# Kernel tuning notes

Hardware: AMD Instinct MI355X
Metric: run time of the kernel (lower is better)

The kernel has to match this reference:

```python
import jax, jax.numpy as jnp
import numpy as np

B, T, D, H, d = 2, 2048, 1024, 16, 64
INNER = H * d
SCALE = d ** -0.5


def _rope(x, inv_freq):
    # x: [B, H, T, d], interleaved rotary as in the torch module
    t = x.shape[2]
    pos = jnp.arange(t, dtype=jnp.float32)
    freqs = pos[:, None] * inv_freq[None, :]          # [T, d/2]
    cos_f, sin_f = jnp.cos(freqs), jnp.sin(freqs)
    x1, x2 = x[..., 0::2], x[..., 1::2]
    y1 = x1 * cos_f - x2 * sin_f
    y2 = x1 * sin_f + x2 * cos_f
    return jnp.stack([y1, y2], axis=-1).reshape(x.shape)


def setup_inputs() -> dict:
    key = jax.random.key(0)
    ks = jax.random.split(key, 6)
    x = jax.random.normal(ks[0], (B, T, D), jnp.float32)
    W_qkv = jax.random.normal(ks[1], (D, 3 * INNER), jnp.float32) * (D ** -0.5)
    W_out = jax.random.normal(ks[2], (INNER, D), jnp.float32) * (INNER ** -0.5)
    W_dt = jax.random.normal(ks[3], (D, H), jnp.float32) * 0.01
    b_dt = jnp.full((H,), -4.0, jnp.float32)
    W_gsp = jax.random.normal(ks[4], (D, INNER), jnp.float32) * 0.01
    b_gsp = jnp.full((INNER,), -3.0, jnp.float32)
    inv_freq = 1.0 / (10000.0 ** (jnp.arange(0, d, 2, dtype=jnp.float32) / d))
    return {"x": x, "W_qkv": W_qkv, "W_out": W_out, "W_dt": W_dt,
            "b_dt": b_dt, "W_gsp": W_gsp, "b_gsp": b_gsp, "inv_freq": inv_freq}


def reference(x, W_qkv, W_out, W_dt, b_dt, W_gsp, b_gsp, inv_freq):
    qkv = (x @ W_qkv).reshape(B, T, 3, H, d)
    Q = jnp.moveaxis(qkv[:, :, 0], 1, 2)   # [B,H,T,d]
    K = jnp.moveaxis(qkv[:, :, 1], 1, 2)
    V = jnp.moveaxis(qkv[:, :, 2], 1, 2)
    Q = _rope(Q, inv_freq)
    K = _rope(K, inv_freq)

    dt = jax.nn.softplus(x @ W_dt + b_dt)             # [B,T,H]
    gamma = jnp.moveaxis(jnp.exp(-dt), 1, 2)          # [B,H,T]

    p = jax.nn.sigmoid(x @ W_gsp + b_gsp).reshape(B, T, H, d)
    p = jnp.moveaxis(p, 1, 2)                          # [B,H,T,d]
    gamma_eff = gamma[..., None] * (1.0 - p) + p
    gamma_scalar = gamma_eff.mean(axis=-1)            # [B,H,T]
    V = V * (1.0 - p)

    log_gamma = jnp.log(jnp.clip(gamma_scalar, 1e-6, 1.0 - 1e-6))
    lgc = jnp.cumsum(log_gamma, axis=-1)              # [B,H,T]
    log_D = jnp.clip(lgc[..., :, None] - lgc[..., None, :], -20.0, 0.0)
    causal = jnp.tril(jnp.ones((T, T), jnp.float32))
    Dm = jnp.exp(log_D) * causal                      # [B,H,T,T]

    Wscore = jnp.einsum('bhtd,bhsd->bhts', Q * SCALE, K)
    A = Wscore * Dm
    Y = jnp.einsum('bhts,bhsd->bhtd', A, V)
    Y = jnp.moveaxis(Y, 1, 2).reshape(B, T, INNER)
    return Y @ W_out
```

## Files before the change

### kernel.cpp

```cpp
#include <hip/hip_runtime.h>
#include <hip/hip_bf16.h>
#include <math.h>

#define B_     2
#define T_     2048
#define D_     1024
#define H_     16
#define INNER_ 1024
#define NC_    4224
#define SCALE_ 0.125f

typedef unsigned short u16;
typedef short short8 __attribute__((ext_vector_type(8)));
typedef float f32x4 __attribute__((ext_vector_type(4)));
typedef unsigned short u16x4 __attribute__((ext_vector_type(4)));

__device__ __forceinline__ u16 f2bf(float x) {
  union { float f; unsigned u; } v; v.f = x;
  unsigned r = v.u + 0x7fffu + ((v.u >> 16) & 1u);
  return (u16)(r >> 16);
}
__device__ __forceinline__ float b2f(u16 x) {
  union { unsigned u; float f; } v; v.u = ((unsigned)x) << 16;
  return v.f;
}
__device__ __forceinline__ void gload16(const void* g, void* l) {
  __builtin_amdgcn_global_load_lds(
      (const __attribute__((address_space(1))) void*)g,
      (__attribute__((address_space(3))) void*)l, 16, 0, 0);
}

__global__ __launch_bounds__(256) void cast_bf16_kernel(
    const float* __restrict__ src, u16* __restrict__ dst, int n4) {
  int i = blockIdx.x * 256 + threadIdx.x;
  if (i >= n4) return;
  float4 v = *reinterpret_cast<const float4*>(src + (size_t)i * 4);
  u16x4 o; o.x = f2bf(v.x); o.y = f2bf(v.y); o.z = f2bf(v.z); o.w = f2bf(v.w);
  *reinterpret_cast<u16x4*>(dst + (size_t)i * 4) = o;
}

__global__ __launch_bounds__(256) void cast_transpose_kernel(
    const float* __restrict__ src, u16* __restrict__ dst, int K, int N) {
  __shared__ float tile[64][65];
  const int k0 = blockIdx.y * 64, n0 = blockIdx.x * 64;
  for (int e = threadIdx.x; e < 4096; e += 256) {
    int kk = e >> 6, nn = e & 63;
    tile[kk][nn] = src[(size_t)(k0 + kk) * N + n0 + nn];
  }
  __syncthreads();
  for (int e = threadIdx.x; e < 4096; e += 256) {
    int nn = e >> 6, kk = e & 63;
    dst[(size_t)(n0 + nn) * K + k0 + kk] = f2bf(tile[kk][nn]);
  }
}

__global__ __launch_bounds__(256) void wdt_transpose_kernel(
    const float* __restrict__ W_dt, u16* __restrict__ dst) {
  int i = blockIdx.x * 256 + threadIdx.x;
  int k = i >> 4, h = i & 15;
  dst[(size_t)h * D_ + k] = f2bf(W_dt[i]);
}

__global__ __launch_bounds__(256) void rope_tab_kernel(
    const float* __restrict__ inv_freq, float2* __restrict__ tab) {
  int i = blockIdx.x * 256 + threadIdx.x;
  int t = i >> 5, j = i & 31;
  float s, c;
  sincosf((float)t * inv_freq[j], &s, &c);
  tab[i] = make_float2(c, s);
}

template <bool BF16OUT>
__global__ __launch_bounds__(256) void gemm_bt(
    const u16* __restrict__ A, const u16* __restrict__ Bt,
    void* __restrict__ Cv, int M, int N, int K) {
  __shared__ u16 As[128 * 64] __attribute__((aligned(16)));
  __shared__ u16 Bs[128 * 64] __attribute__((aligned(16)));
  const int tid = threadIdx.x;
  const int w = tid >> 6, l = tid & 63;
  const int m0 = blockIdx.y * 128, n0 = blockIdx.x * 128;
  const int wr = (w >> 1) * 64, wc = (w & 1) * 64;
  const int srow = l >> 3;
  const int kgrp = ((l & 7) ^ srow) * 8;

  f32x4 acc[4][4] = {};

  for (int kt = 0; kt < K; kt += 64) {
    if (kt) __syncthreads();
#pragma unroll
    for (int i = 0; i < 4; ++i) {
      int c = w * 4 + i;
      int row = c * 8 + srow;
      gload16(A + (size_t)(m0 + row) * K + kt + kgrp, (char*)As + c * 1024);
      gload16(Bt + (size_t)(n0 + row) * K + kt + kgrp, (char*)Bs + c * 1024);
    }
    __syncthreads();
#pragma unroll
    for (int kk = 0; kk < 2; ++kk) {
      short8 af[4], bf[4];
#pragma unroll
      for (int i = 0; i < 4; ++i) {
        int ra = wr + i * 16 + (l & 15);
        int sa = kk * 4 + (l >> 4);
        af[i] = *(const short8*)((const char*)As + ra * 128 + ((sa ^ (ra & 7)) << 4));
        int rb = wc + i * 16 + (l & 15);
        bf[i] = *(const short8*)((const char*)Bs + rb * 128 + ((sa ^ (rb & 7)) << 4));
      }
#pragma unroll
      for (int i = 0; i < 4; ++i)
#pragma unroll
        for (int j = 0; j < 4; ++j)
          acc[i][j] = __builtin_amdgcn_mfma_f32_16x16x32_bf16(af[i], bf[j], acc[i][j], 0, 0, 0);
    }
  }
#pragma unroll
  for (int i = 0; i < 4; ++i) {
#pragma unroll
    for (int r = 0; r < 4; ++r) {
      size_t row = (size_t)(m0 + wr + i * 16 + (l >> 4) * 4 + r);
      size_t base = row * N + n0 + wc + (l & 15);
#pragma unroll
      for (int j = 0; j < 4; ++j) {
        if (BF16OUT) ((u16*)Cv)[base + j * 16] = f2bf(acc[i][j][r]);
        else         ((float*)Cv)[base + j * 16] = acc[i][j][r];
      }
    }
  }
}

__global__ __launch_bounds__(256) void pointwise_kernel(
    const u16* __restrict__ C, const float* __restrict__ b_dt,
    const float* __restrict__ b_gsp, const float2* __restrict__ tab,
    u16* __restrict__ Qb, u16* __restrict__ Kb, u16* __restrict__ Vb,
    float* __restrict__ lg) {
  const int row = blockIdx.x * 4 + (threadIdx.x >> 6);
  const int l = threadIdx.x & 63;
  const int b = row >> 11, t = row & (T_ - 1);
  const int h = l >> 2;
  const int dd0 = (l & 3) * 16;
  const int col = h * 64 + dd0;
  const size_t cb = (size_t)row * NC_;

  float dtv = b2f(C[cb + 4096 + h]) + b_dt[h];
  float sp = (dtv > 20.f) ? dtv : log1pf(__expf(dtv));
  const float gh = __expf(-sp);

  const short8* qp = (const short8*)(C + cb + col);
  const short8* kp = (const short8*)(C + cb + 1024 + col);
  const short8* vp = (const short8*)(C + cb + 2048 + col);
  const short8* pp = (const short8*)(C + cb + 3072 + col);
  short8 q0 = qp[0], q1 = qp[1];
  short8 k0 = kp[0], k1 = kp[1];
  short8 v0 = vp[0], v1 = vp[1];
  short8 pr0 = pp[0], pr1 = pp[1];

  float ge = 0.f;
  short8 vo0, vo1;
#pragma unroll
  for (int i = 0; i < 8; ++i) {
    float pv = b2f((u16)pr0[i]) + b_gsp[col + i];
    float p = 1.f / (1.f + __expf(-pv));
    ge += gh * (1.f - p) + p;
    vo0[i] = (short)f2bf(b2f((u16)v0[i]) * (1.f - p));
    float pv1 = b2f((u16)pr1[i]) + b_gsp[col + 8 + i];
    float p1 = 1.f / (1.f + __expf(-pv1));
    ge += gh * (1.f - p1) + p1;
    vo1[i] = (short)f2bf(b2f((u16)v1[i]) * (1.f - p1));
  }
  const size_t hm = (((size_t)(b * H_ + h)) * T_ + t) * 64 + dd0;
  ((short8*)(Vb + hm))[0] = vo0;
  ((short8*)(Vb + hm))[1] = vo1;

  ge += __shfl_xor(ge, 1);
  ge += __shfl_xor(ge, 2);
  if ((l & 3) == 0) {
    float gs = ge * (1.f / 64.f);
    gs = fminf(fmaxf(gs, 1e-6f), 1.f - 1e-6f);
    lg[((size_t)(b * H_ + h)) * T_ + t] = logf(gs);
  }

  short8 qo0, qo1, ko0, ko1;
  const float2* cs = tab + t * 32 + (dd0 >> 1);
#pragma unroll
  for (int m = 0; m < 4; ++m) {
    float2 c0 = cs[m];
    float qa = b2f((u16)q0[2 * m]), qb = b2f((u16)q0[2 * m + 1]);
    qo0[2 * m]     = (short)f2bf((qa * c0.x - qb * c0.y) * SCALE_);
    qo0[2 * m + 1] = (short)f2bf((qa * c0.y + qb * c0.x) * SCALE_);
    float ka = b2f((u16)k0[2 * m]), kb = b2f((u16)k0[2 * m + 1]);
    ko0[2 * m]     = (short)f2bf(ka * c0.x - kb * c0.y);
    ko0[2 * m + 1] = (short)f2bf(ka * c0.y + kb * c0.x);
    float2 c1 = cs[4 + m];
    float qa1 = b2f((u16)q1[2 * m]), qb1 = b2f((u16)q1[2 * m + 1]);
    qo1[2 * m]     = (short)f2bf((qa1 * c1.x - qb1 * c1.y) * SCALE_);
    qo1[2 * m + 1] = (short)f2bf((qa1 * c1.y + qb1 * c1.x) * SCALE_);
    float ka1 = b2f((u16)k1[2 * m]), kb1 = b2f((u16)k1[2 * m + 1]);
    ko1[2 * m]     = (short)f2bf(ka1 * c1.x - kb1 * c1.y);
    ko1[2 * m + 1] = (short)f2bf(ka1 * c1.y + kb1 * c1.x);
  }
  ((short8*)(Qb + hm))[0] = qo0; ((short8*)(Qb + hm))[1] = qo1;
  ((short8*)(Kb + hm))[0] = ko0; ((short8*)(Kb + hm))[1] = ko1;
}

__global__ __launch_bounds__(256) void scan_kernel(
    const float* __restrict__ lg, float* __restrict__ lgc) {
  const size_t base = (size_t)blockIdx.x * T_;
  const int tid = threadIdx.x;
  __shared__ float sums[256];
  float loc[8];
  float run = 0.f;
#pragma unroll
  for (int i = 0; i < 8; ++i) { run += lg[base + tid * 8 + i]; loc[i] = run; }
  sums[tid] = run;
  __syncthreads();
  if (tid == 0) {
    float r = 0.f;
    for (int i = 0; i < 256; ++i) { float v = sums[i]; sums[i] = r; r += v; }
  }
  __syncthreads();
  const float off = sums[tid];
#pragma unroll
  for (int i = 0; i < 8; ++i) lgc[base + tid * 8 + i] = off + loc[i];
}

__global__ __launch_bounds__(256) void kv_prep_kernel(
    const u16* __restrict__ Kb, const u16* __restrict__ Vb,
    const float* __restrict__ lgc, u16* __restrict__ Kp,
    u16* __restrict__ Vtg) {
  const int stile = blockIdx.x;
  const int bh = blockIdx.y;
  const int tid = threadIdx.x;
  __shared__ u16 vt[64][72];
  const size_t base = ((size_t)bh * T_ + (size_t)stile * 64) * 64;
  const float* lgp = lgc + (size_t)bh * T_;
  const float lgb = lgp[stile * 64];
#pragma unroll
  for (int i = 0; i < 2; ++i) {
    int c = tid * 2 + i;
    int row = c >> 3, k8 = (c & 7) * 8;
    float beta = __expf(lgb - lgp[stile * 64 + row]);
    short8 kv = *(const short8*)(Kb + base + row * 64 + k8);
    short8 ko;
#pragma unroll
    for (int j = 0; j < 8; ++j) ko[j] = (short)f2bf(b2f((u16)kv[j]) * beta);
    *(short8*)(Kp + base + row * 64 + k8) = ko;
    short8 vv = *(const short8*)(Vb + base + row * 64 + k8);
#pragma unroll
    for (int j = 0; j < 8; ++j) vt[row][k8 + j] = (u16)vv[j];
  }
  __syncthreads();
#pragma unroll
  for (int i = 0; i < 2; ++i) {
    int c = tid * 2 + i;
    int dd = c >> 3, t8 = (c & 7) * 8;
    short8 o;
#pragma unroll
    for (int j = 0; j < 8; ++j) o[j] = (short)vt[t8 + j][dd];
    *(short8*)(Vtg + ((size_t)bh * 64 + dd) * T_ + stile * 64 + t8) = o;
  }
}

__global__ __launch_bounds__(256) void attn_mfma(
    const u16* __restrict__ Qb, const u16* __restrict__ Kp,
    const u16* __restrict__ Vtg, const float* __restrict__ lgc,
    u16* __restrict__ Y) {
  const int i = blockIdx.x;
  const int tt = (i >> 3) & 31;
  const int bh = (i & 7) + ((i >> 8) << 3);
  const int b = bh >> 4, h = bh & 15;
  const int tid = threadIdx.x, w = tid >> 6, l = tid & 63;
  __shared__ u16 Qs[64 * 64] __attribute__((aligned(16)));
  __shared__ u16 Ks[64 * 64] __attribute__((aligned(16)));
  __shared__ u16 Vs[64 * 64] __attribute__((aligned(16)));
  const u16* Qg = Qb + (size_t)bh * T_ * 64;
  const u16* Kg = Kp + (size_t)bh * T_ * 64;
  const u16* Vg = Vtg + (size_t)bh * 64 * T_;
  const float* lgp = lgc + (size_t)bh * T_;

  const int srow = l >> 3;
  const int kgrp = ((l & 7) ^ srow) * 8;
  const int ql = l & 15, g4 = l >> 4;

#pragma unroll
  for (int i2 = 0; i2 < 2; ++i2) {
    int c = w * 2 + i2;
    int row = c * 8 + srow;
    gload16(Qg + (size_t)(tt * 64 + row) * 64 + kgrp, (char*)Qs + c * 1024);
  }
  const float lgq = lgp[tt * 64 + w * 16 + ql];
  const float lgtop = lgp[tt * 64];
  __syncthreads();

  short8 qf[2];
#pragma unroll
  for (int kk = 0; kk < 2; ++kk) {
    int row = w * 16 + ql;
    int slot = kk * 4 + g4;
    qf[kk] = *(const short8*)((const char*)Qs + row * 128 + ((slot ^ (row & 7)) << 4));
  }
  char* Pw = (char*)Qs + w * 2048;
  const int pswz = (ql & 7) << 4;

  f32x4 yacc[4] = {};

  for (int st = tt; st >= 0; --st) {
    if (st < tt && lgtop - lgp[st * 64 + 63] <= -20.f) break;
    __syncthreads();
#pragma unroll
    for (int i2 = 0; i2 < 2; ++i2) {
      int c = w * 2 + i2;
      int row = c * 8 + srow;
      gload16(Kg + (size_t)(st * 64 + row) * 64 + kgrp, (char*)Ks + c * 1024);
      gload16(Vg + (size_t)row * T_ + st * 64 + kgrp, (char*)Vs + c * 1024);
    }
    const float alpha = __expf(lgq - lgp[st * 64]);
    __syncthreads();

    const bool diag = (st == tt);
#pragma unroll
    for (int n = 0; n < 4; ++n) {
      f32x4 s = {};
#pragma unroll
      for (int kk = 0; kk < 2; ++kk) {
        int row = n * 16 + ql;
        int slot = kk * 4 + g4;
        short8 kf = *(const short8*)((const char*)Ks + row * 128 + ((slot ^ (row & 7)) << 4));
        s = __builtin_amdgcn_mfma_f32_16x16x32_bf16(kf, qf[kk], s, 0, 0, 0);
      }
      u16x4 pk;
#pragma unroll
      for (int r = 0; r < 4; ++r) {
        float pv = s[r] * alpha;
        if (diag && (n * 16 + g4 * 4 + r) > (w * 16 + ql)) pv = 0.f;
        pk[r] = f2bf(pv);
      }
      *(u16x4*)(Pw + ((ql * 128 + n * 32 + g4 * 8) ^ pswz)) = pk;
    }
#pragma unroll
    for (int kk = 0; kk < 2; ++kk) {
      short8 pf = *(const short8*)(Pw + ((ql * 128 + kk * 64 + g4 * 16) ^ pswz));
#pragma unroll
      for (int n2 = 0; n2 < 4; ++n2) {
        int row = n2 * 16 + ql;
        int slot = kk * 4 + g4;
        short8 vf = *(const short8*)((const char*)Vs + row * 128 + ((slot ^ (row & 7)) << 4));
        yacc[n2] = __builtin_amdgcn_mfma_f32_16x16x32_bf16(pf, vf, yacc[n2], 0, 0, 0);
      }
    }
  }

#pragma unroll
  for (int n2 = 0; n2 < 4; ++n2)
#pragma unroll
    for (int r = 0; r < 4; ++r) {
      size_t row = (size_t)(b * T_) + tt * 64 + w * 16 + g4 * 4 + r;
      Y[row * INNER_ + h * 64 + n2 * 16 + ql] = f2bf(yacc[n2][r]);
    }
}

extern "C" void kernel_launch(void* const* d_in, const int* in_sizes, int n_in,
                              void* d_out, int out_size, void* d_ws, size_t ws_size,
                              hipStream_t stream) {
  const float* x        = (const float*)d_in[0];
  const float* W_qkv    = (const float*)d_in[1];
  const float* W_out    = (const float*)d_in[2];
  const float* W_dt     = (const float*)d_in[3];
  const float* b_dt     = (const float*)d_in[4];
  const float* W_gsp    = (const float*)d_in[5];
  const float* b_gsp    = (const float*)d_in[6];
  const float* inv_freq = (const float*)d_in[7];
  float* out = (float*)d_out;

  const int M = B_ * T_;
  char* p = (char*)d_ws;
  auto alloc = [&](size_t bytes) {
    char* r = p; p += (bytes + 255) & ~(size_t)255; return r;
  };
  u16*    xb    = (u16*)alloc((size_t)M * D_ * 2);
  u16*    Wcombt= (u16*)alloc((size_t)NC_ * D_ * 2);
  u16*    Woutt = (u16*)alloc((size_t)D_ * INNER_ * 2);
  u16*    Cqkvp = (u16*)alloc((size_t)M * NC_ * 2);
  u16*    Qb    = (u16*)alloc((size_t)B_ * H_ * T_ * 64 * 2);
  u16*    Kb    = (u16*)alloc((size_t)B_ * H_ * T_ * 64 * 2);
  u16*    Vb    = (u16*)alloc((size_t)B_ * H_ * T_ * 64 * 2);
  float*  lg    = (float*)alloc((size_t)B_ * H_ * T_ * 4);
  float*  lgc   = (float*)alloc((size_t)B_ * H_ * T_ * 4);
  float2* tab   = (float2*)alloc((size_t)T_ * 32 * 8);
  u16*    Kp    = Cqkvp;
  u16*    Vtg   = Cqkvp + (size_t)4 * 1024 * 1024;
  u16*    Yb    = Cqkvp + (size_t)8 * 1024 * 1024;

  cast_bf16_kernel<<<(M * D_ / 4 + 255) / 256, 256, 0, stream>>>(x, xb, M * D_ / 4);
  rope_tab_kernel<<<T_ * 32 / 256, 256, 0, stream>>>(inv_freq, tab);
  cast_transpose_kernel<<<dim3(3 * INNER_ / 64, D_ / 64), 256, 0, stream>>>(
      W_qkv, Wcombt, D_, 3 * INNER_);
  cast_transpose_kernel<<<dim3(INNER_ / 64, D_ / 64), 256, 0, stream>>>(
      W_gsp, Wcombt + (size_t)3 * INNER_ * D_, D_, INNER_);
  wdt_transpose_kernel<<<64, 256, 0, stream>>>(W_dt, Wcombt + (size_t)4096 * D_);
  cast_transpose_kernel<<<dim3(D_ / 64, INNER_ / 64), 256, 0, stream>>>(
      W_out, Woutt, INNER_, D_);

  gemm_bt<true><<<dim3(NC_ / 128, M / 128), 256, 0, stream>>>(
      xb, Wcombt, Cqkvp, M, NC_, D_);

  pointwise_kernel<<<M / 4, 256, 0, stream>>>(Cqkvp, b_dt, b_gsp, tab,
                                              Qb, Kb, Vb, lg);
  scan_kernel<<<B_ * H_, 256, 0, stream>>>(lg, lgc);
  kv_prep_kernel<<<dim3(T_ / 64, B_ * H_), 256, 0, stream>>>(Kb, Vb, lgc, Kp, Vtg);

  attn_mfma<<<1024, 256, 0, stream>>>(Qb, Kp, Vtg, lgc, Yb);

  gemm_bt<false><<<dim3(D_ / 128, M / 128), 256, 0, stream>>>(
      Yb, Woutt, out, M, D_, INNER_);
}
```

Before: 156.6 us.

## Replace QKV projection GEMM with 256x256-tile pipelined kernel and XCD-aware mapping

Adds a new 512-thread GEMM for the fused QKV/gate/dt projection. It uses 256x256 output tiles, a 4-stage LDS ring buffer fed by global_load_lds with explicit vmcnt waits, swizzled LDS fragments, and a block-to-XCD mapping so each XCD shares A rows. The combined output width is padded from 4224 to 4352 so it splits evenly into 256-wide tiles. This targets load latency and L2 locality in the largest GEMM. In exchange it computes padded extra columns and needs heavy register use (acc 8x4) at occupancy 2.

```diff
diff --git a/kernel.cpp b/kernel.cpp
--- a/kernel.cpp
+++ b/kernel.cpp
@@ -7,7 +7,7 @@
 #define D_     1024
 #define H_     16
 #define INNER_ 1024
-#define NC_    4224
+#define NC_    4352
 #define SCALE_ 0.125f
 
 typedef unsigned short u16;
@@ -68,6 +68,108 @@
   float s, c;
   sincosf((float)t * inv_freq[j], &s, &c);
   tab[i] = make_float2(c, s);
+}
+
+#define SWZG(r) ((((r) & 3) ^ (((r) >> 2) & 1)))
+
+__device__ __forceinline__ void stage_op(const u16* __restrict__ gbase, int kt,
+                                         char* ldst, int h, int tid) {
+  int r = h * 128 + (tid >> 2);
+  int kg = (tid & 3) ^ SWZG(r);
+  gload16(gbase + (size_t)r * D_ + kt * 32 + kg * 8,
+          ldst + (h * 128 + (tid >> 6) * 16) * 64);
+}
+__device__ __forceinline__ short8 ldfrag(const char* tile, int row, int g4) {
+  return *(const short8*)(tile + row * 64 + ((g4 ^ SWZG(row)) << 4));
+}
+
+__global__ __launch_bounds__(512, 2) void gemm_big(
+    const u16* __restrict__ A, const u16* __restrict__ Bt,
+    u16* __restrict__ C) {
+  __shared__ char lds[4 * 32768];
+  const int tid = threadIdx.x;
+  const int w = tid >> 6, l = tid & 63;
+  const int bid = blockIdx.x;
+  const int xcd = bid & 7, j = bid >> 3;
+  const int brow = xcd * 2 + (j >= 17 ? 1 : 0);
+  const int bcol = (j >= 17) ? j - 17 : j;
+  const int m0 = brow * 256, n0 = bcol * 256;
+  const int wr = (w >> 2) * 128, wc = (w & 3) * 64;
+  const int ql = l & 15, g4 = l >> 4;
+
+  const u16* Ag = A + (size_t)m0 * D_;
+  const u16* Bg = Bt + (size_t)n0 * D_;
+
+  f32x4 acc[8][4] = {};
+
+#pragma unroll
+  for (int t = 0; t < 3; ++t) {
+    char* bufA = lds + t * 32768;
+    char* bufB = bufA + 16384;
+    stage_op(Ag, t, bufA, 0, tid); stage_op(Ag, t, bufA, 1, tid);
+    stage_op(Bg, t, bufB, 0, tid); stage_op(Bg, t, bufB, 1, tid);
+  }
+
+  const int NT = D_ / 32;
+  for (int kt = 0; kt < NT; ++kt) {
+    if (kt < NT - 2)       asm volatile("s_waitcnt vmcnt(8)" ::: "memory");
+    else if (kt == NT - 2) asm volatile("s_waitcnt vmcnt(4)" ::: "memory");
+    else                   asm volatile("s_waitcnt vmcnt(0)" ::: "memory");
+    __builtin_amdgcn_sched_barrier(0);
+    __builtin_amdgcn_s_barrier();
+    __builtin_amdgcn_sched_barrier(0);
+
+    char* bufA = lds + (kt & 3) * 32768;
+    char* bufB = bufA + 16384;
+    char* nbufA = lds + ((kt + 3) & 3) * 32768;
+    char* nbufB = nbufA + 16384;
+    const bool pre = (kt + 3 < NT);
+
+    if (pre) {
+      stage_op(Ag, kt + 3, nbufA, 0, tid);
+      stage_op(Ag, kt + 3, nbufA, 1, tid);
+    }
+    short8 bf[4];
+#pragma unroll
+    for (int nf = 0; nf < 4; ++nf) bf[nf] = ldfrag(bufB, wc + nf * 16 + ql, g4);
+    short8 af[4];
+#pragma unroll
+    for (int mf = 0; mf < 4; ++mf) af[mf] = ldfrag(bufA, wr + mf * 16 + ql, g4);
+    __builtin_amdgcn_s_setprio(1);
+#pragma unroll
+    for (int mf = 0; mf < 4; ++mf)
+#pragma unroll
+      for (int nf = 0; nf < 4; ++nf)
+        acc[mf][nf] = __builtin_amdgcn_mfma_f32_16x16x32_bf16(af[mf], bf[nf], acc[mf][nf], 0, 0, 0);
+    __builtin_amdgcn_s_setprio(0);
+
+    if (pre) {
+      stage_op(Bg, kt + 3, nbufB, 0, tid);
+      stage_op(Bg, kt + 3, nbufB, 1, tid);
+    }
+    short8 af2[4];
+#pragma unroll
+    for (int mf = 0; mf < 4; ++mf) af2[mf] = ldfrag(bufA, wr + 64 + mf * 16 + ql, g4);
+    __builtin_amdgcn_s_setprio(1);
+#pragma unroll
+    for (int mf = 0; mf < 4; ++mf)
+#pragma unroll
+      for (int nf = 0; nf < 4; ++nf)
+        acc[mf + 4][nf] = __builtin_amdgcn_mfma_f32_16x16x32_bf16(af2[mf], bf[nf], acc[mf + 4][nf], 0, 0, 0);
+    __builtin_amdgcn_s_setprio(0);
+  }
+
+#pragma unroll
+  for (int mf = 0; mf < 8; ++mf) {
+#pragma unroll
+    for (int r = 0; r < 4; ++r) {
+      size_t row = (size_t)(m0 + wr + mf * 16 + g4 * 4 + r);
+      size_t base = row * NC_ + n0 + wc + ql;
+#pragma unroll
+      for (int nf = 0; nf < 4; ++nf)
+        C[base + nf * 16] = f2bf(acc[mf][nf][r]);
+    }
+  }
 }
 
 template <bool BF16OUT>
@@ -400,8 +502,7 @@
   cast_transpose_kernel<<<dim3(D_ / 64, INNER_ / 64), 256, 0, stream>>>(
       W_out, Woutt, INNER_, D_);
 
-  gemm_bt<true><<<dim3(NC_ / 128, M / 128), 256, 0, stream>>>(
-      xb, Wcombt, Cqkvp, M, NC_, D_);
+  gemm_big<<<272, 512, 0, stream>>>(xb, Wcombt, Cqkvp);
 
   pointwise_kernel<<<M / 4, 256, 0, stream>>>(Cqkvp, b_dt, b_gsp, tab,
                                               Qb, Kb, Vb, lg);
```

Result: slower. 170.0 us (+8.6%).
